# Optimization experiments

Hardware: AMD Instinct MI355X
Metric: run time of the kernel (lower is better)

## Reference

```python
import jax, jax.numpy as jnp
import numpy as np

NUM_EMBEDDINGS = 1024
EMBEDDING_DIM = 128
COMMITMENT_COST = 0.25
B, T = 32, 2048


def setup_inputs() -> dict:
    key = jax.random.key(0)
    k1, k2 = jax.random.split(key)
    inputs = jax.random.normal(k1, (B, T, EMBEDDING_DIM), dtype=jnp.float32)
    lim = 1.0 / NUM_EMBEDDINGS
    embedding_weight = jax.random.uniform(
        k2, (NUM_EMBEDDINGS, EMBEDDING_DIM), dtype=jnp.float32,
        minval=-lim, maxval=lim)
    return {"inputs": inputs, "embedding_weight": embedding_weight}


def reference(inputs, embedding_weight):
    D = embedding_weight.shape[1]
    flat = inputs.reshape(-1, D)                                  # [N, D]
    # squared L2 distances to every codebook entry: [N, K]
    distances = (
        jnp.sum(flat * flat, axis=1, keepdims=True)
        + jnp.sum(embedding_weight * embedding_weight, axis=1)
        - 2.0 * jnp.matmul(flat, embedding_weight.T)
    )
    encoding_indices = jnp.argmin(distances, axis=1)              # [N]
    quantized = embedding_weight[encoding_indices].reshape(inputs.shape)
    sg = jax.lax.stop_gradient
    e_latent_loss = jnp.mean((sg(quantized) - inputs) ** 2)
    q_latent_loss = jnp.mean((quantized - sg(inputs)) ** 2)
    loss = q_latent_loss + COMMITMENT_COST * e_latent_loss
    # straight-through estimator
    quantized = inputs + sg(quantized - inputs)
    return (loss, quantized, encoding_indices)
```

## Files before the change

### kernel.cpp

```cpp
#include <hip/hip_runtime.h>

#define NROWS 65536
#define KC    1024
#define DIM   128
#define W_DIST 5e-5f

typedef short  bf16x8 __attribute__((ext_vector_type(8)));
typedef float  f32x4  __attribute__((ext_vector_type(4)));

__device__ __forceinline__ unsigned short f2bf_rne(float f) {
    unsigned int u = __float_as_uint(f);
    u += 0x7FFFu + ((u >> 16) & 1u);
    return (unsigned short)(u >> 16);
}
__device__ __forceinline__ float bf2f(unsigned short h) {
    return __uint_as_float(((unsigned int)h) << 16);
}

__device__ __forceinline__ void gll16(const unsigned short* g, short* l) {
    __builtin_amdgcn_global_load_lds(
        (const __attribute__((address_space(1))) unsigned int*)g,
        (__attribute__((address_space(3))) unsigned int*)l,
        16, 0, 0);
}

template <int N>
__device__ __forceinline__ void vmwait() {
    if constexpr (N == 4)      asm volatile("s_waitcnt vmcnt(4)" ::: "memory");
    else if constexpr (N == 2) asm volatile("s_waitcnt vmcnt(2)" ::: "memory");
    else                       asm volatile("s_waitcnt vmcnt(0)" ::: "memory");
}

__device__ __forceinline__ float np_sumsq_128(const float* v) {
    float r[8];
    #pragma unroll
    for (int j = 0; j < 8; ++j) r[j] = __fmul_rn(v[j], v[j]);
    #pragma unroll
    for (int i = 1; i < 16; ++i)
        #pragma unroll
        for (int j = 0; j < 8; ++j)
            r[j] = __fadd_rn(r[j], __fmul_rn(v[i * 8 + j], v[i * 8 + j]));
    return __fadd_rn(__fadd_rn(__fadd_rn(r[0], r[1]), __fadd_rn(r[2], r[3])),
                     __fadd_rn(__fadd_rn(r[4], r[5]), __fadd_rn(r[6], r[7])));
}

__global__ __launch_bounds__(256) void vq_prep(const float* __restrict__ emb,
        float* __restrict__ enorm,
        unsigned short* __restrict__ eh, unsigned short* __restrict__ em) {
    const int k = blockIdx.x * 256 + threadIdx.x;
    if (k >= KC) return;
    float v[DIM];
    const float4* e = reinterpret_cast<const float4*>(emb + (size_t)k * DIM);
    #pragma unroll
    for (int i = 0; i < 32; ++i) {
        float4 t = e[i];
        v[i * 4 + 0] = t.x; v[i * 4 + 1] = t.y;
        v[i * 4 + 2] = t.z; v[i * 4 + 3] = t.w;
    }
    enorm[k] = np_sumsq_128(v);
    unsigned short* ph = eh + (size_t)k * DIM;
    unsigned short* pm = em + (size_t)k * DIM;
    #pragma unroll
    for (int i = 0; i < 16; ++i) {
        unsigned int h[8], m[8];
        #pragma unroll
        for (int j = 0; j < 8; ++j) {
            float f = v[i * 8 + j];
            unsigned short hh = f2bf_rne(f);
            h[j] = hh;
            m[j] = f2bf_rne(f - bf2f(hh));
        }
        uint4 vh = {h[0] | (h[1] << 16), h[2] | (h[3] << 16),
                    h[4] | (h[5] << 16), h[6] | (h[7] << 16)};
        uint4 vm = {m[0] | (m[1] << 16), m[2] | (m[3] << 16),
                    m[4] | (m[5] << 16), m[6] | (m[7] << 16)};
        *reinterpret_cast<uint4*>(ph + i * 8) = vh;
        *reinterpret_cast<uint4*>(pm + i * 8) = vm;
    }
}

__global__ __launch_bounds__(256, 2) void vq_mfma(
        const float* __restrict__ x,
        const unsigned short* __restrict__ eh, const unsigned short* __restrict__ em,
        const float* __restrict__ enorm,
        int* __restrict__ bestk, float* __restrict__ idx_out,
        int* __restrict__ fb_cnt, int* __restrict__ fb_rows) {
    const int tid  = threadIdx.x;
    const int lane = tid & 63;
    const int wid  = tid >> 6;
    const int rtile = blockIdx.x * 128 + wid * 32;
    const int lr = lane & 15;
    const int lg = lane >> 4;

    __shared__ short ldsE[4][2][2048];
    __shared__ float s_enorm[KC];

    const int s_row = tid & 15;
    const int s_col = ((tid >> 6) * 32) + (((tid >> 4) & 3) * 8);
    const unsigned short* geh = eh + (size_t)s_row * DIM + s_col;
    const unsigned short* gem = em + (size_t)s_row * DIM + s_col;

#define VQ_STAGE(T)                                                         \
    do {                                                                    \
        const int _b = (T) & 3;                                             \
        gll16(geh + (size_t)(T) * 2048, (short*)&ldsE[_b][0][0] + wid * 512); \
        gll16(gem + (size_t)(T) * 2048, (short*)&ldsE[_b][1][0] + wid * 512); \
    } while (0)

    VQ_STAGE(0); VQ_STAGE(1); VQ_STAGE(2);

    bf16x8 fxh[2][4], fxm[2][4];
    #pragma unroll
    for (int nt = 0; nt < 2; ++nt) {
        const float* px = x + (size_t)(rtile + nt * 16 + lr) * DIM + lg * 8;
        #pragma unroll
        for (int kc = 0; kc < 4; ++kc) {
            float4 a = *reinterpret_cast<const float4*>(px + kc * 32);
            float4 b = *reinterpret_cast<const float4*>(px + kc * 32 + 4);
            float f[8] = {a.x, a.y, a.z, a.w, b.x, b.y, b.z, b.w};
            bf16x8 vh, vm;
            #pragma unroll
            for (int j = 0; j < 8; ++j) {
                unsigned short hh = f2bf_rne(f[j]);
                vh[j] = (short)hh;
                vm[j] = (short)f2bf_rne(f[j] - bf2f(hh));
            }
            fxh[nt][kc] = vh;
            fxm[nt][kc] = vm;
        }
    }
    #pragma unroll
    for (int nt = 0; nt < 2; ++nt)
        #pragma unroll
        for (int kc = 0; kc < 4; ++kc)
            asm volatile("" : "+v"(fxh[nt][kc]), "+v"(fxm[nt][kc]));

    *reinterpret_cast<float4*>(&s_enorm[tid * 4]) =
        *reinterpret_cast<const float4*>(&enorm[tid * 4]);
    __syncthreads();

    float m1_0 = 1e30f, m2_0 = 1e30f; int k1_0 = 0;
    float m1_1 = 1e30f, m2_1 = 1e30f; int k1_1 = 0;

#define VQ_ITER(T, VMN, DO_ISSUE)                                            \
    do {                                                                     \
        vmwait<VMN>();                                                       \
        __builtin_amdgcn_s_barrier();                                        \
        asm volatile("" ::: "memory");                                       \
        const int _buf = (T) & 3;                                            \
        const int _m0 = (T) * 16;                                            \
        const f32x4 nrm = *reinterpret_cast<const f32x4*>(&s_enorm[_m0 + lg * 4]); \
        f32x4 A0 = {0.f,0.f,0.f,0.f}, A1 = {0.f,0.f,0.f,0.f};                \
        f32x4 D0 = {0.f,0.f,0.f,0.f}, D1 = {0.f,0.f,0.f,0.f};                \
        __builtin_amdgcn_s_setprio(1);                                       \
        _Pragma("unroll")                                                    \
        for (int kc = 0; kc < 4; ++kc) {                                     \
            const int off = ((kc * 4 + lg) * 16 + lr) * 8;                   \
            bf16x8 feh = *reinterpret_cast<const bf16x8*>(&ldsE[_buf][0][off]); \
            bf16x8 fem = *reinterpret_cast<const bf16x8*>(&ldsE[_buf][1][off]); \
            A0 = __builtin_amdgcn_mfma_f32_16x16x32_bf16(feh, fxh[0][kc], A0, 0, 0, 0); \
            A1 = __builtin_amdgcn_mfma_f32_16x16x32_bf16(feh, fxh[1][kc], A1, 0, 0, 0); \
            D0 = __builtin_amdgcn_mfma_f32_16x16x32_bf16(feh, fxm[0][kc], D0, 0, 0, 0); \
            D1 = __builtin_amdgcn_mfma_f32_16x16x32_bf16(feh, fxm[1][kc], D1, 0, 0, 0); \
            D0 = __builtin_amdgcn_mfma_f32_16x16x32_bf16(fem, fxh[0][kc], D0, 0, 0, 0); \
            D1 = __builtin_amdgcn_mfma_f32_16x16x32_bf16(fem, fxh[1][kc], D1, 0, 0, 0); \
        }                                                                    \
        __builtin_amdgcn_s_setprio(0);                                       \
        const int kbase = _m0 + lg * 4;                                      \
        _Pragma("unroll")                                                    \
        for (int r = 0; r < 4; ++r) {                                        \
            {   float v = fmaf(-2.0f, A0[r] + D0[r], nrm[r]);                \
                int kk = kbase + r;                                          \
                bool lt = v < m1_0;                                          \
                m2_0 = lt ? m1_0 : fminf(m2_0, v);                           \
                k1_0 = lt ? kk : k1_0;                                       \
                m1_0 = lt ? v : m1_0; }                                      \
            {   float v = fmaf(-2.0f, A1[r] + D1[r], nrm[r]);                \
                int kk = kbase + r;                                          \
                bool lt = v < m1_1;                                          \
                m2_1 = lt ? m1_1 : fminf(m2_1, v);                           \
                k1_1 = lt ? kk : k1_1;                                       \
                m1_1 = lt ? v : m1_1; }                                      \
        }                                                                    \
        if (DO_ISSUE) { VQ_STAGE((T) + 3); }                                 \
    } while (0)

    for (int t = 0; t < 60; ++t) VQ_ITER(t, 4, true);
    VQ_ITER(60, 4, true);
    VQ_ITER(61, 4, false);
    VQ_ITER(62, 2, false);
    VQ_ITER(63, 0, false);
#undef VQ_ITER
#undef VQ_STAGE

    #pragma unroll
    for (int off = 16; off <= 32; off <<= 1) {
        {   float om1 = __shfl_xor(m1_0, off, 64);
            float om2 = __shfl_xor(m2_0, off, 64);
            int   ok1 = __shfl_xor(k1_0, off, 64);
            float hi = fmaxf(m1_0, om1);
            m2_0 = fminf(fminf(m2_0, om2), hi);
            bool take = om1 < m1_0;
            k1_0 = take ? ok1 : k1_0;
            m1_0 = fminf(m1_0, om1); }
        {   float om1 = __shfl_xor(m1_1, off, 64);
            float om2 = __shfl_xor(m2_1, off, 64);
            int   ok1 = __shfl_xor(k1_1, off, 64);
            float hi = fmaxf(m1_1, om1);
            m2_1 = fminf(fminf(m2_1, om2), hi);
            bool take = om1 < m1_1;
            k1_1 = take ? ok1 : k1_1;
            m1_1 = fminf(m1_1, om1); }
    }

    if (lane < 16) {
        #pragma unroll
        for (int nt = 0; nt < 2; ++nt) {
            const int row = rtile + nt * 16 + lane;
            float m1 = nt ? m1_1 : m1_0;
            float m2 = nt ? m2_1 : m2_0;
            int   k1 = nt ? k1_1 : k1_0;
            if (m2 - m1 < W_DIST) {
                int slot = atomicAdd(fb_cnt, 1);
                fb_rows[slot] = row;
            } else {
                bestk[row] = k1;
                idx_out[row] = (float)k1;
            }
        }
    }
}

__global__ __launch_bounds__(512) void vq_fallback(
        const float* __restrict__ x, const float* __restrict__ emb,
        const float* __restrict__ enorm,
        const int* __restrict__ fb_cnt, const int* __restrict__ fb_rows,
        int* __restrict__ bestk, float* __restrict__ idx_out) {
    const int tid  = threadIdx.x;
    const int lane = tid & 63;
    const int wid  = tid >> 6;
    const int nb = *fb_cnt;

    __shared__ float sx[8][DIM];
    __shared__ float s_xn[8];
    __shared__ float swv[8][8];
    __shared__ int   swk[8][8];

    const float en0 = enorm[tid];
    const float en1 = enorm[tid + 512];
    const float4* e0p = reinterpret_cast<const float4*>(emb + (size_t)tid * DIM);
    const float4* e1p = reinterpret_cast<const float4*>(emb + (size_t)(tid + 512) * DIM);

    for (int base = blockIdx.x * 8; base < nb; base += gridDim.x * 8) {
        const int R = min(8, nb - base);
        {
            const int r = tid >> 6;
            const int c2 = (tid & 63) * 2;
            const int slot = fb_rows[min(base + r, nb - 1)];
            float2 v = *reinterpret_cast<const float2*>(x + (size_t)slot * DIM + c2);
            sx[r][c2] = v.x; sx[r][c2 + 1] = v.y;
        }
        __syncthreads();
        if (tid < 8) s_xn[tid] = np_sumsq_128(&sx[tid][0]);
        __syncthreads();

        float a0[8][4], a1[8][4];
        #pragma unroll
        for (int r = 0; r < 8; ++r)
            #pragma unroll
            for (int c = 0; c < 4; ++c) { a0[r][c] = 0.f; a1[r][c] = 0.f; }

        for (int q = 0; q < 32; ++q) {
            float4 ev0 = e0p[q];
            float4 ev1 = e1p[q];
            #pragma unroll
            for (int r = 0; r < 8; ++r) {
                float4 xv = *reinterpret_cast<const float4*>(&sx[r][q * 4]);
                a0[r][0] = fmaf(xv.x, ev0.x, a0[r][0]);
                a0[r][1] = fmaf(xv.y, ev0.y, a0[r][1]);
                a0[r][2] = fmaf(xv.z, ev0.z, a0[r][2]);
                a0[r][3] = fmaf(xv.w, ev0.w, a0[r][3]);
                a1[r][0] = fmaf(xv.x, ev1.x, a1[r][0]);
                a1[r][1] = fmaf(xv.y, ev1.y, a1[r][1]);
                a1[r][2] = fmaf(xv.z, ev1.z, a1[r][2]);
                a1[r][3] = fmaf(xv.w, ev1.w, a1[r][3]);
            }
        }

        float cv[8]; int ck[8];
        #pragma unroll
        for (int r = 0; r < 8; ++r) {
            float xn = s_xn[r];
            float d0 = __fadd_rn(__fadd_rn(a0[r][0], a0[r][1]),
                                 __fadd_rn(a0[r][2], a0[r][3]));
            float s0 = __fsub_rn(__fadd_rn(xn, en0), __fmul_rn(2.0f, d0));
            float d1 = __fadd_rn(__fadd_rn(a1[r][0], a1[r][1]),
                                 __fadd_rn(a1[r][2], a1[r][3]));
            float s1 = __fsub_rn(__fadd_rn(xn, en1), __fmul_rn(2.0f, d1));
            bool t1 = (s1 < s0);
            cv[r] = t1 ? s1 : s0;
            ck[r] = t1 ? tid + 512 : tid;
        }
        #pragma unroll
        for (int off = 1; off < 64; off <<= 1) {
            #pragma unroll
            for (int r = 0; r < 8; ++r) {
                float ov = __shfl_xor(cv[r], off, 64);
                int   ok = __shfl_xor(ck[r], off, 64);
                bool take = (ov < cv[r]) || (ov == cv[r] && ok < ck[r]);
                cv[r] = take ? ov : cv[r];
                ck[r] = take ? ok : ck[r];
            }
        }
        if (lane == 0) {
            #pragma unroll
            for (int r = 0; r < 8; ++r) { swv[wid][r] = cv[r]; swk[wid][r] = ck[r]; }
        }
        __syncthreads();
        if (tid < R) {
            float bv = swv[0][tid]; int bk = swk[0][tid];
            #pragma unroll
            for (int w = 1; w < 8; ++w) {
                float v = swv[w][tid]; int k = swk[w][tid];
                bool take = (v < bv) || (v == bv && k < bk);
                bv = take ? v : bv;
                bk = take ? k : bk;
            }
            const int row = fb_rows[base + tid];
            bestk[row] = bk;
            idx_out[row] = (float)bk;
        }
        __syncthreads();
    }
}

__global__ __launch_bounds__(256) void vq_gather(
        const float* __restrict__ x, const float* __restrict__ emb,
        const int* __restrict__ bestk, float* __restrict__ quant,
        double* __restrict__ partials) {
    const int t = blockIdx.x * 256 + threadIdx.x;
    const int r = t >> 4;
    const int c = (t & 15) * 8;
    const int bk = bestk[r];
    const float4* ep = reinterpret_cast<const float4*>(emb + (size_t)bk * DIM + c);
    const float4* xp = reinterpret_cast<const float4*>(x + (size_t)r * DIM + c);
    float4 e0 = ep[0], e1 = ep[1];
    float4 x0 = xp[0], x1 = xp[1];
    float* q = quant + (size_t)r * DIM + c;
    q[0] = e0.x; q[1] = e0.y; q[2] = e0.z; q[3] = e0.w;
    q[4] = e1.x; q[5] = e1.y; q[6] = e1.z; q[7] = e1.w;
    float d0 = e0.x - x0.x, d1 = e0.y - x0.y, d2 = e0.z - x0.z, d3 = e0.w - x0.w;
    float d4 = e1.x - x1.x, d5 = e1.y - x1.y, d6 = e1.z - x1.z, d7 = e1.w - x1.w;
    float acc = fmaf(d0, d0, fmaf(d1, d1, fmaf(d2, d2, d3 * d3)))
              + fmaf(d4, d4, fmaf(d5, d5, fmaf(d6, d6, d7 * d7)));
    #pragma unroll
    for (int off = 32; off > 0; off >>= 1) acc += __shfl_down(acc, off, 64);

    __shared__ float sacc[4];
    if ((threadIdx.x & 63) == 0) sacc[threadIdx.x >> 6] = acc;
    __syncthreads();
    if (threadIdx.x == 0)
        partials[blockIdx.x] =
            (double)sacc[0] + (double)sacc[1] + (double)sacc[2] + (double)sacc[3];
}

__global__ __launch_bounds__(256) void vq_loss(
        const double* __restrict__ partials, float* __restrict__ out) {
    double s = 0.0;
    #pragma unroll
    for (int i = 0; i < 16; ++i) s += partials[threadIdx.x + i * 256];
    #pragma unroll
    for (int off = 32; off > 0; off >>= 1) s += __shfl_down(s, off, 64);
    __shared__ double sd[4];
    if ((threadIdx.x & 63) == 0) sd[threadIdx.x >> 6] = s;
    __syncthreads();
    if (threadIdx.x == 0)
        out[0] = (float)((sd[0] + sd[1] + sd[2] + sd[3]) * (1.25 / 8388608.0));
}

extern "C" void kernel_launch(void* const* d_in, const int* in_sizes, int n_in,
                              void* d_out, int out_size, void* d_ws, size_t ws_size,
                              hipStream_t stream) {
    const float* x   = (const float*)d_in[0];
    const float* emb = (const float*)d_in[1];

    float* out      = (float*)d_out;
    float* loss_out = out;
    float* quant    = out + 1;
    float* idx_out  = out + 1 + (size_t)NROWS * DIM;

    char* ws = (char*)d_ws;
    int*    fb_cnt   = (int*)(ws + 8);
    float*  enorm    = (float*)(ws + 1024);
    int*    fb_rows  = (int*)(ws + 16384);
    int*    bestk    = (int*)(ws + 278528);
    unsigned short* eh = (unsigned short*)(ws + 557056);
    unsigned short* em = (unsigned short*)(ws + 819200);
    double* partials = (double*)(ws + 1081344);

    hipMemsetAsync(ws, 0, 16, stream);
    vq_prep<<<4, 256, 0, stream>>>(emb, enorm, eh, em);
    vq_mfma<<<512, 256, 0, stream>>>(x, eh, em, enorm,
                                     bestk, idx_out, fb_cnt, fb_rows);
    vq_fallback<<<1024, 512, 0, stream>>>(x, emb, enorm, fb_cnt, fb_rows,
                                          bestk, idx_out);
    vq_gather<<<4096, 256, 0, stream>>>(x, emb, bestk, quant, partials);
    vq_loss<<<1, 256, 0, stream>>>(partials, loss_out);
}
```

Baseline: 113.2 us.

## Switch distance GEMM to 32x32x16 MFMA with deferred argmin epilogue

Replaces the 16x16x32 bf16 MFMA tiles with 32x32x16 tiles. Each wave now covers 32 rows against 32 codes per step, halving the loop trip count, and the codebook staging moves to triple-buffered 32-code chunks. The argmin epilogue for a step is delayed by one iteration using ping-pong accumulators, so the compare/select work overlaps with the next step's MFMAs. The cross-lane reduction shrinks to a single shuffle. The cost is more accumulator registers (four 16-float vectors), which may pressure occupancy at 2 blocks/SM.

```diff
diff --git a/kernel.cpp b/kernel.cpp
--- a/kernel.cpp
+++ b/kernel.cpp
@@ -7,6 +7,9 @@
 
 typedef short  bf16x8 __attribute__((ext_vector_type(8)));
 typedef float  f32x4  __attribute__((ext_vector_type(4)));
+typedef float  f32x16 __attribute__((ext_vector_type(16)));
+
+#define ZERO16 ((f32x16){0.f,0.f,0.f,0.f,0.f,0.f,0.f,0.f,0.f,0.f,0.f,0.f,0.f,0.f,0.f,0.f})
 
 __device__ __forceinline__ unsigned short f2bf_rne(float f) {
     unsigned int u = __float_as_uint(f);
@@ -26,7 +29,8 @@
 
 template <int N>
 __device__ __forceinline__ void vmwait() {
-    if constexpr (N == 4)      asm volatile("s_waitcnt vmcnt(4)" ::: "memory");
+    if constexpr (N == 8)      asm volatile("s_waitcnt vmcnt(8)" ::: "memory");
+    else if constexpr (N == 4) asm volatile("s_waitcnt vmcnt(4)" ::: "memory");
     else if constexpr (N == 2) asm volatile("s_waitcnt vmcnt(2)" ::: "memory");
     else                       asm volatile("s_waitcnt vmcnt(0)" ::: "memory");
 }
@@ -88,35 +92,37 @@
     const int tid  = threadIdx.x;
     const int lane = tid & 63;
     const int wid  = tid >> 6;
+    const int lr31 = lane & 31;
+    const int hi   = lane >> 5;
     const int rtile = blockIdx.x * 128 + wid * 32;
-    const int lr = lane & 15;
-    const int lg = lane >> 4;
-
-    __shared__ short ldsE[4][2][2048];
+
+    __shared__ short ldsE[3][2][4096];
     __shared__ float s_enorm[KC];
 
-    const int s_row = tid & 15;
-    const int s_col = ((tid >> 6) * 32) + (((tid >> 4) & 3) * 8);
-    const unsigned short* geh = eh + (size_t)s_row * DIM + s_col;
-    const unsigned short* gem = em + (size_t)s_row * DIM + s_col;
-
-#define VQ_STAGE(T)                                                         \
+    const int u0 = wid * 128 + lane;
+    const int u1 = wid * 128 + 64 + lane;
+    const int src0 = (u0 & 31) * DIM + (u0 >> 5) * 8;
+    const int src1 = (u1 & 31) * DIM + (u1 >> 5) * 8;
+    const int dst0 = wid * 128 * 8;
+    const int dst1 = (wid * 128 + 64) * 8;
+
+#define VQ_STAGE(T, B)                                                      \
     do {                                                                    \
-        const int _b = (T) & 3;                                             \
-        gll16(geh + (size_t)(T) * 2048, (short*)&ldsE[_b][0][0] + wid * 512); \
-        gll16(gem + (size_t)(T) * 2048, (short*)&ldsE[_b][1][0] + wid * 512); \
+        const unsigned short* _gh = eh + (size_t)(T) * 4096;                \
+        const unsigned short* _gm = em + (size_t)(T) * 4096;                \
+        gll16(_gh + src0, &ldsE[B][0][dst0]);                               \
+        gll16(_gh + src1, &ldsE[B][0][dst1]);                               \
+        gll16(_gm + src0, &ldsE[B][1][dst0]);                               \
+        gll16(_gm + src1, &ldsE[B][1][dst1]);                               \
     } while (0)
 
-    VQ_STAGE(0); VQ_STAGE(1); VQ_STAGE(2);
-
-    bf16x8 fxh[2][4], fxm[2][4];
-    #pragma unroll
-    for (int nt = 0; nt < 2; ++nt) {
-        const float* px = x + (size_t)(rtile + nt * 16 + lr) * DIM + lg * 8;
-        #pragma unroll
-        for (int kc = 0; kc < 4; ++kc) {
-            float4 a = *reinterpret_cast<const float4*>(px + kc * 32);
-            float4 b = *reinterpret_cast<const float4*>(px + kc * 32 + 4);
+    bf16x8 fxh[8], fxm[8];
+    {
+        const float* px = x + (size_t)(rtile + lr31) * DIM + hi * 8;
+        #pragma unroll
+        for (int s = 0; s < 8; ++s) {
+            float4 a = *reinterpret_cast<const float4*>(px + s * 16);
+            float4 b = *reinterpret_cast<const float4*>(px + s * 16 + 4);
             float f[8] = {a.x, a.y, a.z, a.w, b.x, b.y, b.z, b.w};
             bf16x8 vh, vm;
             #pragma unroll
@@ -125,108 +131,104 @@
                 vh[j] = (short)hh;
                 vm[j] = (short)f2bf_rne(f[j] - bf2f(hh));
             }
-            fxh[nt][kc] = vh;
-            fxm[nt][kc] = vm;
-        }
-    }
-    #pragma unroll
-    for (int nt = 0; nt < 2; ++nt)
-        #pragma unroll
-        for (int kc = 0; kc < 4; ++kc)
-            asm volatile("" : "+v"(fxh[nt][kc]), "+v"(fxm[nt][kc]));
+            fxh[s] = vh; fxm[s] = vm;
+        }
+    }
+    #pragma unroll
+    for (int s = 0; s < 8; ++s)
+        asm volatile("" : "+v"(fxh[s]), "+v"(fxm[s]));
 
     *reinterpret_cast<float4*>(&s_enorm[tid * 4]) =
         *reinterpret_cast<const float4*>(&enorm[tid * 4]);
-    __syncthreads();
-
-    float m1_0 = 1e30f, m2_0 = 1e30f; int k1_0 = 0;
-    float m1_1 = 1e30f, m2_1 = 1e30f; int k1_1 = 0;
-
-#define VQ_ITER(T, VMN, DO_ISSUE)                                            \
-    do {                                                                     \
-        vmwait<VMN>();                                                       \
-        __builtin_amdgcn_s_barrier();                                        \
-        asm volatile("" ::: "memory");                                       \
-        const int _buf = (T) & 3;                                            \
-        const int _m0 = (T) * 16;                                            \
-        const f32x4 nrm = *reinterpret_cast<const f32x4*>(&s_enorm[_m0 + lg * 4]); \
-        f32x4 A0 = {0.f,0.f,0.f,0.f}, A1 = {0.f,0.f,0.f,0.f};                \
-        f32x4 D0 = {0.f,0.f,0.f,0.f}, D1 = {0.f,0.f,0.f,0.f};                \
-        __builtin_amdgcn_s_setprio(1);                                       \
-        _Pragma("unroll")                                                    \
-        for (int kc = 0; kc < 4; ++kc) {                                     \
-            const int off = ((kc * 4 + lg) * 16 + lr) * 8;                   \
-            bf16x8 feh = *reinterpret_cast<const bf16x8*>(&ldsE[_buf][0][off]); \
-            bf16x8 fem = *reinterpret_cast<const bf16x8*>(&ldsE[_buf][1][off]); \
-            A0 = __builtin_amdgcn_mfma_f32_16x16x32_bf16(feh, fxh[0][kc], A0, 0, 0, 0); \
-            A1 = __builtin_amdgcn_mfma_f32_16x16x32_bf16(feh, fxh[1][kc], A1, 0, 0, 0); \
-            D0 = __builtin_amdgcn_mfma_f32_16x16x32_bf16(feh, fxm[0][kc], D0, 0, 0, 0); \
-            D1 = __builtin_amdgcn_mfma_f32_16x16x32_bf16(feh, fxm[1][kc], D1, 0, 0, 0); \
-            D0 = __builtin_amdgcn_mfma_f32_16x16x32_bf16(fem, fxh[0][kc], D0, 0, 0, 0); \
-            D1 = __builtin_amdgcn_mfma_f32_16x16x32_bf16(fem, fxh[1][kc], D1, 0, 0, 0); \
-        }                                                                    \
-        __builtin_amdgcn_s_setprio(0);                                       \
-        const int kbase = _m0 + lg * 4;                                      \
-        _Pragma("unroll")                                                    \
-        for (int r = 0; r < 4; ++r) {                                        \
-            {   float v = fmaf(-2.0f, A0[r] + D0[r], nrm[r]);                \
-                int kk = kbase + r;                                          \
-                bool lt = v < m1_0;                                          \
-                m2_0 = lt ? m1_0 : fminf(m2_0, v);                           \
-                k1_0 = lt ? kk : k1_0;                                       \
-                m1_0 = lt ? v : m1_0; }                                      \
-            {   float v = fmaf(-2.0f, A1[r] + D1[r], nrm[r]);                \
-                int kk = kbase + r;                                          \
-                bool lt = v < m1_1;                                          \
-                m2_1 = lt ? m1_1 : fminf(m2_1, v);                           \
-                k1_1 = lt ? kk : k1_1;                                       \
-                m1_1 = lt ? v : m1_1; }                                      \
-        }                                                                    \
-        if (DO_ISSUE) { VQ_STAGE((T) + 3); }                                 \
+
+    VQ_STAGE(0, 0);
+    VQ_STAGE(1, 1);
+
+    asm volatile("s_waitcnt lgkmcnt(0)" ::: "memory");
+    __builtin_amdgcn_s_barrier();
+
+    float m1 = 1e30f, m2 = 1e30f; int k1 = 0;
+    f32x16 aE, dE, aO, dO;
+
+#define VQ_EPI(T, PA, PD)                                                   \
+    do {                                                                    \
+        const int _kb = (T) * 32 + (hi << 2);                               \
+        _Pragma("unroll")                                                   \
+        for (int g = 0; g < 4; ++g) {                                       \
+            const f32x4 _nr = *reinterpret_cast<const f32x4*>(&s_enorm[_kb + g * 8]); \
+            _Pragma("unroll")                                               \
+            for (int j = 0; j < 4; ++j) {                                   \
+                const int _r = g * 4 + j;                                   \
+                float _v = fmaf(-2.0f, PA[_r] + PD[_r], _nr[j]);            \
+                int _kk = _kb + g * 8 + j;                                  \
+                bool _lt = _v < m1;                                         \
+                m2 = fminf(m2, fmaxf(m1, _v));                              \
+                k1 = _lt ? _kk : k1;                                        \
+                m1 = fminf(m1, _v);                                         \
+            }                                                               \
+        }                                                                   \
     } while (0)
 
-    for (int t = 0; t < 60; ++t) VQ_ITER(t, 4, true);
-    VQ_ITER(60, 4, true);
-    VQ_ITER(61, 4, false);
-    VQ_ITER(62, 2, false);
-    VQ_ITER(63, 0, false);
+#define VQ_ITER(T, B, SB, CA, CD, PA, PD, VMN, DOSTAGE, DOEPI)              \
+    do {                                                                    \
+        vmwait<VMN>();                                                      \
+        __builtin_amdgcn_s_barrier();                                       \
+        asm volatile("" ::: "memory");                                      \
+        CA = ZERO16; CD = ZERO16;                                           \
+        __builtin_amdgcn_s_setprio(1);                                      \
+        _Pragma("unroll")                                                   \
+        for (int s = 0; s < 8; ++s) {                                       \
+            const int _u = ((s * 2 + hi) * 32 + lr31) * 8;                  \
+            bf16x8 feh = *reinterpret_cast<const bf16x8*>(&ldsE[B][0][_u]); \
+            bf16x8 fem = *reinterpret_cast<const bf16x8*>(&ldsE[B][1][_u]); \
+            CA = __builtin_amdgcn_mfma_f32_32x32x16_bf16(feh, fxh[s], CA, 0, 0, 0); \
+            CD = __builtin_amdgcn_mfma_f32_32x32x16_bf16(feh, fxm[s], CD, 0, 0, 0); \
+            CD = __builtin_amdgcn_mfma_f32_32x32x16_bf16(fem, fxh[s], CD, 0, 0, 0); \
+        }                                                                   \
+        __builtin_amdgcn_s_setprio(0);                                      \
+        if (DOSTAGE) { VQ_STAGE((T) + 2, SB); }                             \
+        if (DOEPI)   { VQ_EPI((T) - 1, PA, PD); }                           \
+    } while (0)
+
+    VQ_ITER(0, 0, 2, aE, dE, aO, dO, 4, 1, 0);
+    VQ_ITER(1, 1, 0, aO, dO, aE, dE, 4, 1, 1);
+    VQ_ITER(2, 2, 1, aE, dE, aO, dO, 4, 1, 1);
+    VQ_ITER(3, 0, 2, aO, dO, aE, dE, 4, 1, 1);
+    VQ_ITER(4, 1, 0, aE, dE, aO, dO, 4, 1, 1);
+    VQ_ITER(5, 2, 1, aO, dO, aE, dE, 4, 1, 1);
+    for (int tb = 6; tb < 30; tb += 6) {
+        VQ_ITER(tb + 0, 0, 2, aE, dE, aO, dO, 4, 1, 1);
+        VQ_ITER(tb + 1, 1, 0, aO, dO, aE, dE, 4, 1, 1);
+        VQ_ITER(tb + 2, 2, 1, aE, dE, aO, dO, 4, 1, 1);
+        VQ_ITER(tb + 3, 0, 2, aO, dO, aE, dE, 4, 1, 1);
+        VQ_ITER(tb + 4, 1, 0, aE, dE, aO, dO, 4, 1, 1);
+        VQ_ITER(tb + 5, 2, 1, aO, dO, aE, dE, 4, 1, 1);
+    }
+    VQ_ITER(30, 0, 2, aE, dE, aO, dO, 4, 0, 1);
+    VQ_ITER(31, 1, 0, aO, dO, aE, dE, 0, 0, 1);
+    VQ_EPI(31, aO, dO);
 #undef VQ_ITER
+#undef VQ_EPI
 #undef VQ_STAGE
 
-    #pragma unroll
-    for (int off = 16; off <= 32; off <<= 1) {
-        {   float om1 = __shfl_xor(m1_0, off, 64);
-            float om2 = __shfl_xor(m2_0, off, 64);
-            int   ok1 = __shfl_xor(k1_0, off, 64);
-            float hi = fmaxf(m1_0, om1);
-            m2_0 = fminf(fminf(m2_0, om2), hi);
-            bool take = om1 < m1_0;
-            k1_0 = take ? ok1 : k1_0;
-            m1_0 = fminf(m1_0, om1); }
-        {   float om1 = __shfl_xor(m1_1, off, 64);
-            float om2 = __shfl_xor(m2_1, off, 64);
-            int   ok1 = __shfl_xor(k1_1, off, 64);
-            float hi = fmaxf(m1_1, om1);
-            m2_1 = fminf(fminf(m2_1, om2), hi);
-            bool take = om1 < m1_1;
-            k1_1 = take ? ok1 : k1_1;
-            m1_1 = fminf(m1_1, om1); }
-    }
-
-    if (lane < 16) {
-        #pragma unroll
-        for (int nt = 0; nt < 2; ++nt) {
-            const int row = rtile + nt * 16 + lane;
-            float m1 = nt ? m1_1 : m1_0;
-            float m2 = nt ? m2_1 : m2_0;
-            int   k1 = nt ? k1_1 : k1_0;
-            if (m2 - m1 < W_DIST) {
-                int slot = atomicAdd(fb_cnt, 1);
-                fb_rows[slot] = row;
-            } else {
-                bestk[row] = k1;
-                idx_out[row] = (float)k1;
-            }
+    {
+        float om1 = __shfl_xor(m1, 32, 64);
+        float om2 = __shfl_xor(m2, 32, 64);
+        int   ok1 = __shfl_xor(k1, 32, 64);
+        float mx = fmaxf(m1, om1);
+        m2 = fminf(fminf(m2, om2), mx);
+        bool take = (om1 < m1) || (om1 == m1 && ok1 < k1);
+        k1 = take ? ok1 : k1;
+        m1 = fminf(m1, om1);
+    }
+    if (lane < 32) {
+        const int row = rtile + lane;
+        if (m2 - m1 < W_DIST) {
+            int slot = atomicAdd(fb_cnt, 1);
+            fb_rows[slot] = row;
+        } else {
+            bestk[row] = k1;
+            idx_out[row] = (float)k1;
         }
     }
 }
```

Result: faster. 110.4 us (-2.5%).
